# Kernel optimization log

Hardware: AMD Instinct MI355X
Metric: run time of the kernel (lower is better)

## Reference

```python
import jax, jax.numpy as jnp
import numpy as np

B, S, D, F, E = 8, 8192, 256, 1024, 8
ROUTE_KEY = 42  # fixed seed replacing torch's Categorical(...).sample()


def setup_inputs() -> dict:
    key = jax.random.key(0)
    ks = jax.random.split(key, 8)
    scale = 0.02
    return {
        "x": jax.random.normal(ks[0], (B, S, D), dtype=jnp.float32),
        "gate_w": jax.random.normal(ks[1], (D, E), dtype=jnp.float32) * scale,
        "gate_b": jnp.zeros((E,), dtype=jnp.float32),
        "w1": jax.random.normal(ks[2], (E, D, F), dtype=jnp.float32) * scale,
        "b1": jnp.zeros((E, F), dtype=jnp.float32),
        "w2": jax.random.normal(ks[3], (E, F, D), dtype=jnp.float32) * scale,
        "b2": jnp.zeros((E, D), dtype=jnp.float32),
    }


def reference(x, gate_w, gate_b, w1, b1, w2, b2):
    # Gate: logits -> softmax -> sample one expert per token.
    # (softmax is monotonic-preserving for categorical sampling, so sampling
    # from logits directly matches Categorical(softmax(logits)).sample().)
    gate_logits = jnp.einsum("bsd,de->bse", x, gate_w) + gate_b
    chosen = jax.random.categorical(jax.random.key(ROUTE_KEY), gate_logits)  # [B,S] int

    num_experts = w1.shape[0]
    out = jnp.zeros_like(x)
    for e in range(num_experts):  # small fixed expert count
        h = jax.nn.relu(jnp.einsum("bsd,df->bsf", x, w1[e]) + b1[e])
        y = jnp.einsum("bsf,fd->bsd", h, w2[e]) + b2[e]
        # scatter-write rows routed to expert e (dropout is identity in eval)
        out = out + jnp.where((chosen == e)[..., None], y, jnp.zeros((), x.dtype))
    return out
```

## Files before the change

### kernel.cpp

```cpp
#include <hip/hip_runtime.h>
#include <hip/hip_bf16.h>

#define NTOK 65536
#define DD 256
#define FF 1024
#define EE 8
#define BSTRIDE 12288
#define MTILE 128
#define NTILES (BSTRIDE / MTILE)
#define CHUNK_US 16384

typedef short bh8 __attribute__((ext_vector_type(8)));
typedef float f16v __attribute__((ext_vector_type(16)));

__device__ __forceinline__ unsigned rotl32(unsigned v, int d) {
  return (v << d) | (v >> (32 - d));
}

__device__ __forceinline__ unsigned jax_random_bits32(unsigned c0, unsigned c1) {
  const unsigned k0 = 0u, k1 = 42u;
  const unsigned k2 = 0x1BD11BDAu ^ k0 ^ k1;
  unsigned x0 = c0 + k0, x1 = c1 + k1;
#define TFR(r) { x0 += x1; x1 = rotl32(x1, (r)); x1 ^= x0; }
  TFR(13) TFR(15) TFR(26) TFR(6)
  x0 += k1; x1 += k2 + 1u;
  TFR(17) TFR(29) TFR(16) TFR(24)
  x0 += k2; x1 += k0 + 2u;
  TFR(13) TFR(15) TFR(26) TFR(6)
  x0 += k0; x1 += k1 + 3u;
  TFR(17) TFR(29) TFR(16) TFR(24)
  x0 += k1; x1 += k2 + 4u;
  TFR(13) TFR(15) TFR(26) TFR(6)
  x0 += k2; x1 += k0 + 5u;
#undef TFR
  return x0 ^ x1;
}

__device__ __forceinline__ ushort f2bf(float f) {
  union { float f; unsigned u; } c; c.f = f;
  unsigned r = c.u + 0x7fffu + ((c.u >> 16) & 1u);
  return (ushort)(r >> 16);
}

__device__ __forceinline__ unsigned pack2(float a, float b) {
  return (unsigned)f2bf(a) | ((unsigned)f2bf(b) << 16);
}

__global__ __launch_bounds__(1024) void gate_route3(
    const float* __restrict__ x, const float* __restrict__ gw,
    const float* __restrict__ gb, int* __restrict__ counts,
    int* __restrict__ buckets, ushort* __restrict__ xbf) {
  __shared__ float gwt[EE * DD];
  __shared__ int hist[EE], sbase[EE];
  __shared__ unsigned char chs[64];
  __shared__ short lps[64];

  const int tid = threadIdx.x;
  if (tid < EE) hist[tid] = 0;
  for (int i = tid; i < DD * EE; i += 1024) {
    const int d = i >> 3, e = i & 7;
    gwt[e * DD + d] = gw[i];
  }
  __syncthreads();

  const int lane = tid & 63;
  const int wave = tid >> 6;
  const int grp = lane >> 4;
  const int gl = lane & 15;
  const int slot = wave * 4 + grp;
  const int t = blockIdx.x * 64 + slot;

  float acc[EE] = {0.f, 0.f, 0.f, 0.f, 0.f, 0.f, 0.f, 0.f};
  const float* xr = x + (size_t)t * DD;
#pragma unroll
  for (int j = 0; j < 4; ++j) {
    const int d0 = j * 64 + gl * 4;
    const float4 xv = *reinterpret_cast<const float4*>(xr + d0);
    if (xbf != nullptr) {
      ushort4 xb;
      xb.x = f2bf(xv.x); xb.y = f2bf(xv.y); xb.z = f2bf(xv.z); xb.w = f2bf(xv.w);
      *reinterpret_cast<ushort4*>(xbf + (size_t)t * DD + d0) = xb;
    }
#pragma unroll
    for (int e = 0; e < EE; ++e) {
      const float4 g = *reinterpret_cast<const float4*>(&gwt[e * DD + d0]);
      acc[e] = fmaf(xv.x, g.x, acc[e]);
      acc[e] = fmaf(xv.y, g.y, acc[e]);
      acc[e] = fmaf(xv.z, g.z, acc[e]);
      acc[e] = fmaf(xv.w, g.w, acc[e]);
    }
  }
#pragma unroll
  for (int off = 8; off >= 1; off >>= 1)
#pragma unroll
    for (int e = 0; e < EE; ++e) acc[e] += __shfl_xor(acc[e], off);

  const int e = gl & 7;
  float logit = 0.f;
#pragma unroll
  for (int q = 0; q < EE; ++q) logit = (e == q) ? acc[q] : logit;
  logit += gb[e];

  const unsigned bits = jax_random_bits32(0u, (unsigned)(t * EE + e));
  const float f = __uint_as_float((bits >> 9) | 0x3f800000u) - 1.0f;
  const float u = fmaxf(1.17549435e-38f, f);
  float val = -logf(-logf(u)) + logit;
  int idx = e;
#pragma unroll
  for (int off = 4; off > 0; off >>= 1) {
    const float ov = __shfl_xor(val, off);
    const int oi = __shfl_xor(idx, off);
    if (ov > val || (ov == val && oi < idx)) { val = ov; idx = oi; }
  }
  if (gl == 0) {
    const int lp = atomicAdd(&hist[idx], 1);
    chs[slot] = (unsigned char)idx;
    lps[slot] = (short)lp;
  }
  __syncthreads();
  if (tid < EE) sbase[tid] = atomicAdd(&counts[tid], hist[tid]);
  __syncthreads();
  if (tid < 64) {
    const int ee = chs[tid];
    const int p = sbase[ee] + lps[tid];
    if (p < BSTRIDE) buckets[ee * BSTRIDE + p] = blockIdx.x * 64 + tid;
  }
}

__global__ __launch_bounds__(256) void prep_w1s(
    const float* __restrict__ w1, ushort* __restrict__ w1s) {
  __shared__ float ts[64][65];
  const int e = blockIdx.z;
  const int f0 = blockIdx.x * 64, d0 = blockIdx.y * 64;
  const int tx = threadIdx.x, ty = threadIdx.y;
  const float* s = w1 + (size_t)e * DD * FF;
  char* dimg = (char*)(w1s + (size_t)e * 16 * CHUNK_US + blockIdx.x * CHUNK_US);
#pragma unroll
  for (int i = 0; i < 16; ++i)
    ts[ty * 16 + i][tx] = s[(size_t)(d0 + ty * 16 + i) * FF + f0 + tx];
  __syncthreads();
#pragma unroll
  for (int i = 0; i < 16; ++i) {
    const int fl = ty * 16 + i;
    const int byte = ((fl * 512 + (d0 + tx) * 2)) ^ ((fl & 31) << 4);
    *reinterpret_cast<ushort*>(dimg + byte) = f2bf(ts[tx][fl]);
  }
}

__global__ __launch_bounds__(256) void prep_w2s(
    const float* __restrict__ w2, ushort* __restrict__ w2s) {
  __shared__ float ts[64][65];
  const int e = blockIdx.z;
  const int d0 = blockIdx.x * 64, f0 = blockIdx.y * 64;
  const int tx = threadIdx.x, ty = threadIdx.y;
  const float* s = w2 + (size_t)e * FF * DD;
  char* dimg = (char*)(w2s + (size_t)e * 16 * CHUNK_US + blockIdx.y * CHUNK_US);
#pragma unroll
  for (int i = 0; i < 16; ++i)
    ts[ty * 16 + i][tx] = s[(size_t)(f0 + ty * 16 + i) * DD + d0 + tx];
  __syncthreads();
#pragma unroll
  for (int i = 0; i < 16; ++i) {
    const int d = d0 + ty * 16 + i;
    const int byte = ((d * 128 + tx * 2)) ^ ((d & 31) << 4);
    *reinterpret_cast<ushort*>(dimg + byte) = f2bf(ts[tx][ty * 16 + i]);
  }
}

__device__ __forceinline__ void stage32k(const ushort* g, ushort* l, int wid, int lane) {
  const ushort* gs = g + wid * 2048 + lane * 8;
  ushort* ls = l + wid * 2048;
#pragma unroll
  for (int i = 0; i < 4; ++i)
    __builtin_amdgcn_global_load_lds(
        (const __attribute__((address_space(1))) void*)(gs + i * 512),
        (__attribute__((address_space(3))) void*)(ls + i * 512), 16, 0, 0);
}

__global__ __launch_bounds__(512, 2) void ffn_mfma7(
    const ushort* __restrict__ xbf, const ushort* __restrict__ w1s,
    const float* __restrict__ b1, const ushort* __restrict__ w2s,
    const float* __restrict__ b2, const int* __restrict__ counts,
    const int* __restrict__ buckets, float* __restrict__ out) {
  const int e = blockIdx.x & 7;
  const int tile = blockIdx.x >> 3;
  const int cnt = min(counts[e], BSTRIDE);
  const int m0 = tile * MTILE;
  if (m0 >= cnt) return;

  __shared__ ushort W1b[2][CHUNK_US];
  __shared__ ushort W2b[2][CHUNK_US];
  __shared__ ushort Hb[8192];
  __shared__ int toks[MTILE];

  const int tid = threadIdx.x;
  const int lane = tid & 63;
  const int wid = tid >> 6;
  const int l31 = lane & 31;
  const int h = lane >> 5;
  const int g = wid & 1;
  const int j = wid >> 1;
  const int mh = wid >> 2;
  const int dq = wid & 3;

  if (tid < MTILE) {
    const int i = m0 + tid;
    toks[tid] = buckets[e * BSTRIDE + (i < cnt ? i : cnt - 1)];
  }

  const ushort* w1g = w1s + (size_t)e * 16 * CHUNK_US;
  const ushort* w2g = w2s + (size_t)e * 16 * CHUNK_US;

  stage32k(w1g, W1b[0], wid, lane);
  stage32k(w2g, W2b[0], wid, lane);

  const int mx = m0 + j * 32 + l31;
  const int tokx = buckets[e * BSTRIDE + (mx < cnt ? mx : cnt - 1)];
  const ushort* xp = xbf + (size_t)tokx * DD + h * 8;
  bh8 xf[16];
#pragma unroll
  for (int ks = 0; ks < 16; ++ks)
    xf[ks] = *reinterpret_cast<const bh8*>(xp + ks * 16);

  const int fl = g * 32 + l31;
  const int w1x = (fl & 31) << 4;
  __syncthreads();

  f16v yacc[2][2] = {};

#pragma unroll 1
  for (int c = 0; c < 16; ++c) {
    const int p = c & 1;
    if (c < 15) {
      stage32k(w1g + (size_t)(c + 1) * CHUNK_US, W1b[p ^ 1], wid, lane);
      stage32k(w2g + (size_t)(c + 1) * CHUNK_US, W2b[p ^ 1], wid, lane);
    }

    {
      const char* wb = reinterpret_cast<const char*>(W1b[p]);
      f16v hacc = {};
#pragma unroll
      for (int ks = 0; ks < 16; ++ks) {
        const int byte = (fl * 512 + ks * 32 + h * 16) ^ w1x;
        const bh8 a = *reinterpret_cast<const bh8*>(wb + byte);
        hacc = __builtin_amdgcn_mfma_f32_32x32x16_bf16(a, xf[ks], hacc, 0, 0, 0);
      }
      float hv[16];
#pragma unroll
      for (int q = 0; q < 4; ++q) {
        const float4 bv = *reinterpret_cast<const float4*>(
            b1 + e * FF + c * 64 + g * 32 + q * 8 + 4 * h);
        hv[q * 4 + 0] = fmaxf(hacc[q * 4 + 0] + bv.x, 0.f);
        hv[q * 4 + 1] = fmaxf(hacc[q * 4 + 1] + bv.y, 0.f);
        hv[q * 4 + 2] = fmaxf(hacc[q * 4 + 2] + bv.z, 0.f);
        hv[q * 4 + 3] = fmaxf(hacc[q * 4 + 3] + bv.w, 0.f);
      }
      char* hbb = reinterpret_cast<char*>(Hb);
#pragma unroll
      for (int ksl = 0; ksl < 2; ++ksl) {
        const unsigned plo0 = pack2(hv[8 * ksl + 0], hv[8 * ksl + 1]);
        const unsigned plo1 = pack2(hv[8 * ksl + 2], hv[8 * ksl + 3]);
        const unsigned phi0 = pack2(hv[8 * ksl + 4], hv[8 * ksl + 5]);
        const unsigned phi1 = pack2(hv[8 * ksl + 6], hv[8 * ksl + 7]);
        const unsigned r0 = (unsigned)__shfl_xor((int)(h ? plo0 : phi0), 32);
        const unsigned r1 = (unsigned)__shfl_xor((int)(h ? plo1 : phi1), 32);
        uint4 w;
        w.x = h ? r0 : plo0;
        w.y = h ? r1 : plo1;
        w.z = h ? phi0 : r0;
        w.w = h ? phi1 : r1;
        const int M = j, K = g * 2 + ksl;
        *reinterpret_cast<uint4*>(hbb + (M * 4 + K) * 1024 + lane * 16) = w;
      }
    }
    __syncthreads();

    {
      const char* hbb = reinterpret_cast<const char*>(Hb);
      const char* wb = reinterpret_cast<const char*>(W2b[p]);
#pragma unroll
      for (int K = 0; K < 4; ++K) {
        const bh8 a0 = *reinterpret_cast<const bh8*>(
            hbb + ((mh * 2 + 0) * 4 + K) * 1024 + lane * 16);
        const bh8 a1 = *reinterpret_cast<const bh8*>(
            hbb + ((mh * 2 + 1) * 4 + K) * 1024 + lane * 16);
#pragma unroll
        for (int dt = 0; dt < 2; ++dt) {
          const int d = dq * 64 + dt * 32 + l31;
          const int byte = (d * 128 + K * 32 + h * 16) ^ ((d & 31) << 4);
          const bh8 b = *reinterpret_cast<const bh8*>(wb + byte);
          yacc[0][dt] = __builtin_amdgcn_mfma_f32_32x32x16_bf16(a0, b, yacc[0][dt], 0, 0, 0);
          yacc[1][dt] = __builtin_amdgcn_mfma_f32_32x32x16_bf16(a1, b, yacc[1][dt], 0, 0, 0);
        }
      }
    }
    __syncthreads();
  }

#pragma unroll
  for (int mb = 0; mb < 2; ++mb) {
#pragma unroll
    for (int dt = 0; dt < 2; ++dt) {
      const int d = dq * 64 + dt * 32 + l31;
      const float b2v = b2[e * DD + d];
#pragma unroll
      for (int r = 0; r < 16; ++r) {
        const int m = mh * 64 + mb * 32 + (r & 3) + 8 * (r >> 2) + 4 * h;
        if (m0 + m < cnt) {
          out[(size_t)toks[m] * DD + d] = yacc[mb][dt][r] + b2v;
        }
      }
    }
  }
}

__global__ __launch_bounds__(512) void ffn_fp32(
    const float* __restrict__ x, const float* __restrict__ w1,
    const float* __restrict__ b1, const float* __restrict__ w2,
    const float* __restrict__ b2, const int* __restrict__ counts,
    const int* __restrict__ buckets, float* __restrict__ out, int bstride) {
  const int e = blockIdx.y;
  const int cnt = min(counts[e], bstride);
  const int m0 = blockIdx.x * 64;
  if (m0 >= cnt) return;

  __shared__ float Xt[DD][64];
  __shared__ float Ht[64][64];
  __shared__ int toks[64];

  const int tid = threadIdx.x;
  if (tid < 64) {
    const int i = m0 + tid;
    toks[tid] = buckets[e * bstride + (i < cnt ? i : cnt - 1)];
  }
  __syncthreads();

  for (int idx = tid; idx < 64 * (DD / 4); idx += 512) {
    const int r = idx >> 6;
    const int c4 = idx & 63;
    const float4 v = *reinterpret_cast<const float4*>(x + (size_t)toks[r] * DD + c4 * 4);
    Xt[c4 * 4 + 0][r] = v.x;
    Xt[c4 * 4 + 1][r] = v.y;
    Xt[c4 * 4 + 2][r] = v.z;
    Xt[c4 * 4 + 3][r] = v.w;
  }
  __syncthreads();

  const int fg = tid & 15;
  const int mg = tid >> 4;
  const int dc = tid & 63;
  const int mgrp = tid >> 6;

  float yacc[8][4];
#pragma unroll
  for (int i = 0; i < 8; ++i)
#pragma unroll
    for (int jj = 0; jj < 4; ++jj) yacc[i][jj] = 0.f;

  for (int fc0 = 0; fc0 < FF; fc0 += 64) {
    float hacc[2][4];
#pragma unroll
    for (int i = 0; i < 2; ++i)
#pragma unroll
      for (int jj = 0; jj < 4; ++jj) hacc[i][jj] = 0.f;

    const float* w1p = w1 + (size_t)e * DD * FF + fc0 + fg * 4;
    for (int d = 0; d < DD; ++d) {
      const float4 w = *reinterpret_cast<const float4*>(w1p + (size_t)d * FF);
      const float2 xv = *reinterpret_cast<const float2*>(&Xt[d][mg * 2]);
      const float ws[4] = {w.x, w.y, w.z, w.w};
      const float xl[2] = {xv.x, xv.y};
#pragma unroll
      for (int i = 0; i < 2; ++i)
#pragma unroll
        for (int jj = 0; jj < 4; ++jj)
          hacc[i][jj] = fmaf(xl[i], ws[jj], hacc[i][jj]);
    }
#pragma unroll
    for (int jj = 0; jj < 4; ++jj) {
      const float bb = b1[e * FF + fc0 + fg * 4 + jj];
      Ht[fg * 4 + jj][mg * 2 + 0] = fmaxf(hacc[0][jj] + bb, 0.f);
      Ht[fg * 4 + jj][mg * 2 + 1] = fmaxf(hacc[1][jj] + bb, 0.f);
    }
    __syncthreads();

    const float* w2p = w2 + (size_t)e * FF * DD + (size_t)fc0 * DD + dc * 4;
    for (int f = 0; f < 64; ++f) {
      const float4 w = *reinterpret_cast<const float4*>(w2p + (size_t)f * DD);
      const float4 h0 = *reinterpret_cast<const float4*>(&Ht[f][mgrp * 8]);
      const float4 h1 = *reinterpret_cast<const float4*>(&Ht[f][mgrp * 8 + 4]);
      const float hs[8] = {h0.x, h0.y, h0.z, h0.w, h1.x, h1.y, h1.z, h1.w};
      const float ws[4] = {w.x, w.y, w.z, w.w};
#pragma unroll
      for (int i = 0; i < 8; ++i)
#pragma unroll
        for (int jj = 0; jj < 4; ++jj)
          yacc[i][jj] = fmaf(hs[i], ws[jj], yacc[i][jj]);
    }
    __syncthreads();
  }

#pragma unroll
  for (int i = 0; i < 8; ++i) {
    const int r = mgrp * 8 + i;
    if (m0 + r < cnt) {
      float4 o;
      o.x = yacc[i][0] + b2[e * DD + dc * 4 + 0];
      o.y = yacc[i][1] + b2[e * DD + dc * 4 + 1];
      o.z = yacc[i][2] + b2[e * DD + dc * 4 + 2];
      o.w = yacc[i][3] + b2[e * DD + dc * 4 + 3];
      *reinterpret_cast<float4*>(out + (size_t)toks[r] * DD + dc * 4) = o;
    }
  }
}

extern "C" void kernel_launch(void* const* d_in, const int* in_sizes, int n_in,
                              void* d_out, int out_size, void* d_ws, size_t ws_size,
                              hipStream_t stream) {
  const float* x  = (const float*)d_in[0];
  const float* gw = (const float*)d_in[1];
  const float* gb = (const float*)d_in[2];
  const float* w1 = (const float*)d_in[3];
  const float* b1 = (const float*)d_in[4];
  const float* w2 = (const float*)d_in[5];
  const float* b2 = (const float*)d_in[6];
  float* out = (float*)d_out;

  int* counts = (int*)d_ws;
  int* buckets = (int*)((char*)d_ws + 4096);
  ushort* w1s = (ushort*)((char*)d_ws + 524288);
  ushort* w2s = (ushort*)((char*)d_ws + 524288 + 4194304);
  ushort* xbf = (ushort*)((char*)d_ws + 524288 + 2ull * 4194304);
  const size_t need = 524288 + 2ull * 4194304 + (size_t)NTOK * DD * 2;

  hipMemsetAsync(d_ws, 0, 4096, stream);

  if (ws_size >= need) {
    hipLaunchKernelGGL(gate_route3, dim3(NTOK / 64), dim3(1024), 0, stream,
                       x, gw, gb, counts, buckets, xbf);
    hipLaunchKernelGGL(prep_w1s, dim3(FF / 64, DD / 64, EE), dim3(64, 4), 0, stream,
                       w1, w1s);
    hipLaunchKernelGGL(prep_w2s, dim3(DD / 64, FF / 64, EE), dim3(64, 4), 0, stream,
                       w2, w2s);
    hipLaunchKernelGGL(ffn_mfma7, dim3(NTILES * EE), dim3(512), 0, stream,
                       xbf, w1s, b1, w2s, b2, counts, buckets, out);
  } else {
    hipLaunchKernelGGL(gate_route3, dim3(NTOK / 64), dim3(1024), 0, stream,
                       x, gw, gb, counts, buckets, (ushort*)nullptr);
    hipLaunchKernelGGL(ffn_fp32, dim3(NTOK / 64, EE), dim3(512), 0, stream,
                       x, w1, b1, w2, b2, counts, buckets, out, BSTRIDE);
  }
}
```

Measured before the change: 181.9 us.

## Warp-specialize FFN kernel into GEMM1 producer and GEMM2 consumer wave groups

Splits the eight waves into two groups. Four waves compute the first GEMM plus ReLU for chunk c+1 while the other four run the second GEMM for chunk c, passing H through double-buffered shared memory. The row tile shrinks from 128 to 64 tokens, which doubles the number of blocks. b1 is cached in shared memory, and s_setprio is raised around the MFMA loops. Halving the tile also doubles how often each block rereads the weights and limits each GEMM to half the waves, so the overlap gain may be offset by more weight traffic.

```diff
diff --git a/kernel.cpp b/kernel.cpp
--- a/kernel.cpp
+++ b/kernel.cpp
@@ -6,7 +6,7 @@
 #define FF 1024
 #define EE 8
 #define BSTRIDE 12288
-#define MTILE 128
+#define MTILE 64
 #define NTILES (BSTRIDE / MTILE)
 #define CHUNK_US 16384
 
@@ -167,17 +167,17 @@
   }
 }
 
-__device__ __forceinline__ void stage32k(const ushort* g, ushort* l, int wid, int lane) {
-  const ushort* gs = g + wid * 2048 + lane * 8;
-  ushort* ls = l + wid * 2048;
-#pragma unroll
-  for (int i = 0; i < 4; ++i)
+__device__ __forceinline__ void stage32k4(const ushort* g, ushort* l, int widx, int lane) {
+  const ushort* gs = g + widx * 4096 + lane * 8;
+  ushort* ls = l + widx * 4096;
+#pragma unroll
+  for (int i = 0; i < 8; ++i)
     __builtin_amdgcn_global_load_lds(
         (const __attribute__((address_space(1))) void*)(gs + i * 512),
         (__attribute__((address_space(3))) void*)(ls + i * 512), 16, 0, 0);
 }
 
-__global__ __launch_bounds__(512, 2) void ffn_mfma7(
+__global__ __launch_bounds__(512, 2) void ffn_pc(
     const ushort* __restrict__ xbf, const ushort* __restrict__ w1s,
     const float* __restrict__ b1, const ushort* __restrict__ w2s,
     const float* __restrict__ b2, const int* __restrict__ counts,
@@ -190,7 +190,8 @@
 
   __shared__ ushort W1b[2][CHUNK_US];
   __shared__ ushort W2b[2][CHUNK_US];
-  __shared__ ushort Hb[8192];
+  __shared__ ushort Hb[2][4096];
+  __shared__ float Bb[FF];
   __shared__ int toks[MTILE];
 
   const int tid = threadIdx.x;
@@ -198,117 +199,134 @@
   const int wid = tid >> 6;
   const int l31 = lane & 31;
   const int h = lane >> 5;
-  const int g = wid & 1;
-  const int j = wid >> 1;
-  const int mh = wid >> 2;
-  const int dq = wid & 3;
+  const bool isG1 = (wid < 4);
+  const int g = wid >> 1;
+  const int j = wid & 1;
+  const int w2i = wid - 4;
+  const int mh = w2i >> 1;
+  const int dq = w2i & 1;
 
   if (tid < MTILE) {
     const int i = m0 + tid;
     toks[tid] = buckets[e * BSTRIDE + (i < cnt ? i : cnt - 1)];
   }
+  Bb[tid] = b1[e * FF + tid];
+  Bb[tid + 512] = b1[e * FF + 512 + tid];
 
   const ushort* w1g = w1s + (size_t)e * 16 * CHUNK_US;
   const ushort* w2g = w2s + (size_t)e * 16 * CHUNK_US;
 
-  stage32k(w1g, W1b[0], wid, lane);
-  stage32k(w2g, W2b[0], wid, lane);
-
-  const int mx = m0 + j * 32 + l31;
-  const int tokx = buckets[e * BSTRIDE + (mx < cnt ? mx : cnt - 1)];
-  const ushort* xp = xbf + (size_t)tokx * DD + h * 8;
+  if (isG1) {
+    stage32k4(w1g, W1b[0], wid, lane);
+    stage32k4(w1g + CHUNK_US, W1b[1], wid, lane);
+  } else {
+    stage32k4(w2g, W2b[0], w2i, lane);
+  }
+
   bh8 xf[16];
-#pragma unroll
-  for (int ks = 0; ks < 16; ++ks)
-    xf[ks] = *reinterpret_cast<const bh8*>(xp + ks * 16);
+  if (isG1) {
+    const int mxi = m0 + j * 32 + l31;
+    const int tokx = buckets[e * BSTRIDE + (mxi < cnt ? mxi : cnt - 1)];
+    const ushort* xp = xbf + (size_t)tokx * DD + h * 8;
+#pragma unroll
+    for (int ks = 0; ks < 16; ++ks)
+      xf[ks] = *reinterpret_cast<const bh8*>(xp + ks * 16);
+  }
 
   const int fl = g * 32 + l31;
   const int w1x = (fl & 31) << 4;
-  __syncthreads();
-
-  f16v yacc[2][2] = {};
+
+  __syncthreads();
+
+  auto g1_compute = [&](int cc) {
+    const char* wb = reinterpret_cast<const char*>(W1b[cc & 1]);
+    f16v hacc = {};
+    __builtin_amdgcn_s_setprio(1);
+#pragma unroll
+    for (int ks = 0; ks < 16; ++ks) {
+      const int byte = (fl * 512 + ks * 32 + h * 16) ^ w1x;
+      const bh8 a = *reinterpret_cast<const bh8*>(wb + byte);
+      hacc = __builtin_amdgcn_mfma_f32_32x32x16_bf16(a, xf[ks], hacc, 0, 0, 0);
+    }
+    __builtin_amdgcn_s_setprio(0);
+    float hv[16];
+#pragma unroll
+    for (int q = 0; q < 4; ++q) {
+      const float4 bv = *reinterpret_cast<const float4*>(
+          &Bb[cc * 64 + g * 32 + q * 8 + 4 * h]);
+      hv[q * 4 + 0] = fmaxf(hacc[q * 4 + 0] + bv.x, 0.f);
+      hv[q * 4 + 1] = fmaxf(hacc[q * 4 + 1] + bv.y, 0.f);
+      hv[q * 4 + 2] = fmaxf(hacc[q * 4 + 2] + bv.z, 0.f);
+      hv[q * 4 + 3] = fmaxf(hacc[q * 4 + 3] + bv.w, 0.f);
+    }
+    char* hbb = reinterpret_cast<char*>(Hb[cc & 1]);
+#pragma unroll
+    for (int ksl = 0; ksl < 2; ++ksl) {
+      const unsigned plo0 = pack2(hv[8 * ksl + 0], hv[8 * ksl + 1]);
+      const unsigned plo1 = pack2(hv[8 * ksl + 2], hv[8 * ksl + 3]);
+      const unsigned phi0 = pack2(hv[8 * ksl + 4], hv[8 * ksl + 5]);
+      const unsigned phi1 = pack2(hv[8 * ksl + 6], hv[8 * ksl + 7]);
+      const unsigned r0 = (unsigned)__shfl_xor((int)(h ? plo0 : phi0), 32);
+      const unsigned r1 = (unsigned)__shfl_xor((int)(h ? plo1 : phi1), 32);
+      uint4 w;
+      w.x = h ? r0 : plo0;
+      w.y = h ? r1 : plo1;
+      w.z = h ? phi0 : r0;
+      w.w = h ? phi1 : r1;
+      const int K = g * 2 + ksl;
+      *reinterpret_cast<uint4*>(hbb + (j * 4 + K) * 1024 + lane * 16) = w;
+    }
+  };
+
+  f16v yacc[4] = {};
+
+  auto g2_compute = [&](int c) {
+    const char* hbb = reinterpret_cast<const char*>(Hb[c & 1]);
+    const char* wb = reinterpret_cast<const char*>(W2b[c & 1]);
+    __builtin_amdgcn_s_setprio(1);
+#pragma unroll
+    for (int K = 0; K < 4; ++K) {
+      const bh8 hfa = *reinterpret_cast<const bh8*>(
+          hbb + ((mh * 4 + K) * 64 + lane) * 16);
+#pragma unroll
+      for (int dt = 0; dt < 4; ++dt) {
+        const int d = dq * 128 + dt * 32 + l31;
+        const int byte = (d * 128 + K * 32 + h * 16) ^ ((d & 31) << 4);
+        const bh8 b = *reinterpret_cast<const bh8*>(wb + byte);
+        yacc[dt] = __builtin_amdgcn_mfma_f32_32x32x16_bf16(hfa, b, yacc[dt], 0, 0, 0);
+      }
+    }
+    __builtin_amdgcn_s_setprio(0);
+  };
+
+  if (isG1) g1_compute(0);
+  __syncthreads();
 
 #pragma unroll 1
   for (int c = 0; c < 16; ++c) {
-    const int p = c & 1;
-    if (c < 15) {
-      stage32k(w1g + (size_t)(c + 1) * CHUNK_US, W1b[p ^ 1], wid, lane);
-      stage32k(w2g + (size_t)(c + 1) * CHUNK_US, W2b[p ^ 1], wid, lane);
-    }
-
-    {
-      const char* wb = reinterpret_cast<const char*>(W1b[p]);
-      f16v hacc = {};
-#pragma unroll
-      for (int ks = 0; ks < 16; ++ks) {
-        const int byte = (fl * 512 + ks * 32 + h * 16) ^ w1x;
-        const bh8 a = *reinterpret_cast<const bh8*>(wb + byte);
-        hacc = __builtin_amdgcn_mfma_f32_32x32x16_bf16(a, xf[ks], hacc, 0, 0, 0);
-      }
-      float hv[16];
-#pragma unroll
-      for (int q = 0; q < 4; ++q) {
-        const float4 bv = *reinterpret_cast<const float4*>(
-            b1 + e * FF + c * 64 + g * 32 + q * 8 + 4 * h);
-        hv[q * 4 + 0] = fmaxf(hacc[q * 4 + 0] + bv.x, 0.f);
-        hv[q * 4 + 1] = fmaxf(hacc[q * 4 + 1] + bv.y, 0.f);
-        hv[q * 4 + 2] = fmaxf(hacc[q * 4 + 2] + bv.z, 0.f);
-        hv[q * 4 + 3] = fmaxf(hacc[q * 4 + 3] + bv.w, 0.f);
-      }
-      char* hbb = reinterpret_cast<char*>(Hb);
-#pragma unroll
-      for (int ksl = 0; ksl < 2; ++ksl) {
-        const unsigned plo0 = pack2(hv[8 * ksl + 0], hv[8 * ksl + 1]);
-        const unsigned plo1 = pack2(hv[8 * ksl + 2], hv[8 * ksl + 3]);
-        const unsigned phi0 = pack2(hv[8 * ksl + 4], hv[8 * ksl + 5]);
-        const unsigned phi1 = pack2(hv[8 * ksl + 6], hv[8 * ksl + 7]);
-        const unsigned r0 = (unsigned)__shfl_xor((int)(h ? plo0 : phi0), 32);
-        const unsigned r1 = (unsigned)__shfl_xor((int)(h ? plo1 : phi1), 32);
-        uint4 w;
-        w.x = h ? r0 : plo0;
-        w.y = h ? r1 : plo1;
-        w.z = h ? phi0 : r0;
-        w.w = h ? phi1 : r1;
-        const int M = j, K = g * 2 + ksl;
-        *reinterpret_cast<uint4*>(hbb + (M * 4 + K) * 1024 + lane * 16) = w;
-      }
+    if (isG1) {
+      if (c + 2 < 16)
+        stage32k4(w1g + (size_t)(c + 2) * CHUNK_US, W1b[c & 1], wid, lane);
+      if (c + 1 < 16)
+        g1_compute(c + 1);
+    } else {
+      if (c + 1 < 16)
+        stage32k4(w2g + (size_t)(c + 1) * CHUNK_US, W2b[(c + 1) & 1], w2i, lane);
+      g2_compute(c);
     }
     __syncthreads();
-
-    {
-      const char* hbb = reinterpret_cast<const char*>(Hb);
-      const char* wb = reinterpret_cast<const char*>(W2b[p]);
-#pragma unroll
-      for (int K = 0; K < 4; ++K) {
-        const bh8 a0 = *reinterpret_cast<const bh8*>(
-            hbb + ((mh * 2 + 0) * 4 + K) * 1024 + lane * 16);
-        const bh8 a1 = *reinterpret_cast<const bh8*>(
-            hbb + ((mh * 2 + 1) * 4 + K) * 1024 + lane * 16);
-#pragma unroll
-        for (int dt = 0; dt < 2; ++dt) {
-          const int d = dq * 64 + dt * 32 + l31;
-          const int byte = (d * 128 + K * 32 + h * 16) ^ ((d & 31) << 4);
-          const bh8 b = *reinterpret_cast<const bh8*>(wb + byte);
-          yacc[0][dt] = __builtin_amdgcn_mfma_f32_32x32x16_bf16(a0, b, yacc[0][dt], 0, 0, 0);
-          yacc[1][dt] = __builtin_amdgcn_mfma_f32_32x32x16_bf16(a1, b, yacc[1][dt], 0, 0, 0);
-        }
-      }
-    }
-    __syncthreads();
-  }
-
-#pragma unroll
-  for (int mb = 0; mb < 2; ++mb) {
-#pragma unroll
-    for (int dt = 0; dt < 2; ++dt) {
-      const int d = dq * 64 + dt * 32 + l31;
+  }
+
+  if (!isG1) {
+#pragma unroll
+    for (int dt = 0; dt < 4; ++dt) {
+      const int d = dq * 128 + dt * 32 + l31;
       const float b2v = b2[e * DD + d];
 #pragma unroll
       for (int r = 0; r < 16; ++r) {
-        const int m = mh * 64 + mb * 32 + (r & 3) + 8 * (r >> 2) + 4 * h;
-        if (m0 + m < cnt) {
-          out[(size_t)toks[m] * DD + d] = yacc[mb][dt][r] + b2v;
-        }
+        const int m = mh * 32 + (r & 3) + 8 * (r >> 2) + 4 * h;
+        if (m0 + m < cnt)
+          out[(size_t)toks[m] * DD + d] = yacc[dt][r] + b2v;
       }
     }
   }
@@ -442,7 +460,7 @@
                        w1, w1s);
     hipLaunchKernelGGL(prep_w2s, dim3(DD / 64, FF / 64, EE), dim3(64, 4), 0, stream,
                        w2, w2s);
-    hipLaunchKernelGGL(ffn_mfma7, dim3(NTILES * EE), dim3(512), 0, stream,
+    hipLaunchKernelGGL(ffn_pc, dim3(NTILES * EE), dim3(512), 0, stream,
                        xbf, w1s, b1, w2s, b2, counts, buckets, out);
   } else {
     hipLaunchKernelGGL(gate_route3, dim3(NTOK / 64), dim3(1024), 0, stream,
```

Measured after the change: 208.0 us. 1.14x slower.

## Split FFN chunk loop into phased pipeline with staggered prefetch and barriers

Applied to the files above, without the earlier changes.

Restructures the per-chunk loop of the expert FFN kernel into five phases (two half-GEMM1, pack, two half-GEMM2), each separated by a light barrier. The next chunk's weight prefetches are spread across the phases, with explicit vmcnt waits in place of full syncthreads. It also raises wave priority around the MFMA bursts and moves b1 into shared memory. The aim is to overlap global-to-LDS staging with matrix work and cut barrier stalls, at the cost of more barriers and fragile hand-tuned wait counts.

```diff
diff --git a/kernel.cpp b/kernel.cpp
--- a/kernel.cpp
+++ b/kernel.cpp
@@ -12,6 +12,12 @@
 
 typedef short bh8 __attribute__((ext_vector_type(8)));
 typedef float f16v __attribute__((ext_vector_type(16)));
+
+#define PHASE_BAR() do { \
+  asm volatile("s_waitcnt lgkmcnt(0)" ::: "memory"); \
+  __builtin_amdgcn_s_barrier(); \
+  __builtin_amdgcn_sched_barrier(0); \
+} while (0)
 
 __device__ __forceinline__ unsigned rotl32(unsigned v, int d) {
   return (v << d) | (v >> (32 - d));
@@ -176,8 +182,17 @@
         (const __attribute__((address_space(1))) void*)(gs + i * 512),
         (__attribute__((address_space(3))) void*)(ls + i * 512), 16, 0, 0);
 }
-
-__global__ __launch_bounds__(512, 2) void ffn_mfma7(
+__device__ __forceinline__ void stage16k(const ushort* g, ushort* l, int wid, int lane, int half) {
+  const ushort* gs = g + wid * 2048 + lane * 8;
+  ushort* ls = l + wid * 2048;
+#pragma unroll
+  for (int i = 2 * half; i < 2 * half + 2; ++i)
+    __builtin_amdgcn_global_load_lds(
+        (const __attribute__((address_space(1))) void*)(gs + i * 512),
+        (__attribute__((address_space(3))) void*)(ls + i * 512), 16, 0, 0);
+}
+
+__global__ __launch_bounds__(512, 2) void ffn_8p(
     const ushort* __restrict__ xbf, const ushort* __restrict__ w1s,
     const float* __restrict__ b1, const ushort* __restrict__ w2s,
     const float* __restrict__ b2, const int* __restrict__ counts,
@@ -191,6 +206,7 @@
   __shared__ ushort W1b[2][CHUNK_US];
   __shared__ ushort W2b[2][CHUNK_US];
   __shared__ ushort Hb[8192];
+  __shared__ float Bb[FF];
   __shared__ int toks[MTILE];
 
   const int tid = threadIdx.x;
@@ -207,6 +223,8 @@
     const int i = m0 + tid;
     toks[tid] = buckets[e * BSTRIDE + (i < cnt ? i : cnt - 1)];
   }
+  Bb[tid] = b1[e * FF + tid];
+  Bb[tid + 512] = b1[e * FF + 512 + tid];
 
   const ushort* w1g = w1s + (size_t)e * 16 * CHUNK_US;
   const ushort* w2g = w2s + (size_t)e * 16 * CHUNK_US;
@@ -228,73 +246,106 @@
 
   f16v yacc[2][2] = {};
 
+  auto g1_half = [&](const char* wb, bh8* xfp, f16v& hacc, int k0) {
+    __builtin_amdgcn_s_setprio(1);
+#pragma unroll
+    for (int ks = 0; ks < 8; ++ks) {
+      const int kk = k0 + ks;
+      const int byte = (fl * 512 + kk * 32 + h * 16) ^ w1x;
+      const bh8 a = *reinterpret_cast<const bh8*>(wb + byte);
+      hacc = __builtin_amdgcn_mfma_f32_32x32x16_bf16(a, xfp[kk], hacc, 0, 0, 0);
+    }
+    __builtin_amdgcn_s_setprio(0);
+  };
+
+  auto h_pack = [&](int cc, const f16v& hacc) {
+    float hv[16];
+#pragma unroll
+    for (int q = 0; q < 4; ++q) {
+      const float4 bv = *reinterpret_cast<const float4*>(
+          &Bb[cc * 64 + g * 32 + q * 8 + 4 * h]);
+      hv[q * 4 + 0] = fmaxf(hacc[q * 4 + 0] + bv.x, 0.f);
+      hv[q * 4 + 1] = fmaxf(hacc[q * 4 + 1] + bv.y, 0.f);
+      hv[q * 4 + 2] = fmaxf(hacc[q * 4 + 2] + bv.z, 0.f);
+      hv[q * 4 + 3] = fmaxf(hacc[q * 4 + 3] + bv.w, 0.f);
+    }
+    char* hbb = reinterpret_cast<char*>(Hb);
+#pragma unroll
+    for (int ksl = 0; ksl < 2; ++ksl) {
+      const unsigned plo0 = pack2(hv[8 * ksl + 0], hv[8 * ksl + 1]);
+      const unsigned plo1 = pack2(hv[8 * ksl + 2], hv[8 * ksl + 3]);
+      const unsigned phi0 = pack2(hv[8 * ksl + 4], hv[8 * ksl + 5]);
+      const unsigned phi1 = pack2(hv[8 * ksl + 6], hv[8 * ksl + 7]);
+      const unsigned r0 = (unsigned)__shfl_xor((int)(h ? plo0 : phi0), 32);
+      const unsigned r1 = (unsigned)__shfl_xor((int)(h ? plo1 : phi1), 32);
+      uint4 w;
+      w.x = h ? r0 : plo0;
+      w.y = h ? r1 : plo1;
+      w.z = h ? phi0 : r0;
+      w.w = h ? phi1 : r1;
+      const int K = g * 2 + ksl;
+      *reinterpret_cast<uint4*>(hbb + (j * 4 + K) * 1024 + lane * 16) = w;
+    }
+  };
+
+  auto g2_half = [&](const char* wb, int K0) {
+    const char* hbb = reinterpret_cast<const char*>(Hb);
+    __builtin_amdgcn_s_setprio(1);
+#pragma unroll
+    for (int Ki = 0; Ki < 2; ++Ki) {
+      const int K = K0 + Ki;
+      const bh8 a0 = *reinterpret_cast<const bh8*>(
+          hbb + ((mh * 2 + 0) * 4 + K) * 1024 + lane * 16);
+      const bh8 a1 = *reinterpret_cast<const bh8*>(
+          hbb + ((mh * 2 + 1) * 4 + K) * 1024 + lane * 16);
+#pragma unroll
+      for (int dt = 0; dt < 2; ++dt) {
+        const int d = dq * 64 + dt * 32 + l31;
+        const int byte = (d * 128 + K * 32 + h * 16) ^ ((d & 31) << 4);
+        const bh8 b = *reinterpret_cast<const bh8*>(wb + byte);
+        yacc[0][dt] = __builtin_amdgcn_mfma_f32_32x32x16_bf16(a0, b, yacc[0][dt], 0, 0, 0);
+        yacc[1][dt] = __builtin_amdgcn_mfma_f32_32x32x16_bf16(a1, b, yacc[1][dt], 0, 0, 0);
+      }
+    }
+    __builtin_amdgcn_s_setprio(0);
+  };
+
 #pragma unroll 1
-  for (int c = 0; c < 16; ++c) {
+  for (int c = 0; c < 15; ++c) {
     const int p = c & 1;
-    if (c < 15) {
-      stage32k(w1g + (size_t)(c + 1) * CHUNK_US, W1b[p ^ 1], wid, lane);
-      stage32k(w2g + (size_t)(c + 1) * CHUNK_US, W2b[p ^ 1], wid, lane);
-    }
-
-    {
-      const char* wb = reinterpret_cast<const char*>(W1b[p]);
-      f16v hacc = {};
-#pragma unroll
-      for (int ks = 0; ks < 16; ++ks) {
-        const int byte = (fl * 512 + ks * 32 + h * 16) ^ w1x;
-        const bh8 a = *reinterpret_cast<const bh8*>(wb + byte);
-        hacc = __builtin_amdgcn_mfma_f32_32x32x16_bf16(a, xf[ks], hacc, 0, 0, 0);
-      }
-      float hv[16];
-#pragma unroll
-      for (int q = 0; q < 4; ++q) {
-        const float4 bv = *reinterpret_cast<const float4*>(
-            b1 + e * FF + c * 64 + g * 32 + q * 8 + 4 * h);
-        hv[q * 4 + 0] = fmaxf(hacc[q * 4 + 0] + bv.x, 0.f);
-        hv[q * 4 + 1] = fmaxf(hacc[q * 4 + 1] + bv.y, 0.f);
-        hv[q * 4 + 2] = fmaxf(hacc[q * 4 + 2] + bv.z, 0.f);
-        hv[q * 4 + 3] = fmaxf(hacc[q * 4 + 3] + bv.w, 0.f);
-      }
-      char* hbb = reinterpret_cast<char*>(Hb);
-#pragma unroll
-      for (int ksl = 0; ksl < 2; ++ksl) {
-        const unsigned plo0 = pack2(hv[8 * ksl + 0], hv[8 * ksl + 1]);
-        const unsigned plo1 = pack2(hv[8 * ksl + 2], hv[8 * ksl + 3]);
-        const unsigned phi0 = pack2(hv[8 * ksl + 4], hv[8 * ksl + 5]);
-        const unsigned phi1 = pack2(hv[8 * ksl + 6], hv[8 * ksl + 7]);
-        const unsigned r0 = (unsigned)__shfl_xor((int)(h ? plo0 : phi0), 32);
-        const unsigned r1 = (unsigned)__shfl_xor((int)(h ? plo1 : phi1), 32);
-        uint4 w;
-        w.x = h ? r0 : plo0;
-        w.y = h ? r1 : plo1;
-        w.z = h ? phi0 : r0;
-        w.w = h ? phi1 : r1;
-        const int M = j, K = g * 2 + ksl;
-        *reinterpret_cast<uint4*>(hbb + (M * 4 + K) * 1024 + lane * 16) = w;
-      }
-    }
-    __syncthreads();
-
-    {
-      const char* hbb = reinterpret_cast<const char*>(Hb);
-      const char* wb = reinterpret_cast<const char*>(W2b[p]);
-#pragma unroll
-      for (int K = 0; K < 4; ++K) {
-        const bh8 a0 = *reinterpret_cast<const bh8*>(
-            hbb + ((mh * 2 + 0) * 4 + K) * 1024 + lane * 16);
-        const bh8 a1 = *reinterpret_cast<const bh8*>(
-            hbb + ((mh * 2 + 1) * 4 + K) * 1024 + lane * 16);
-#pragma unroll
-        for (int dt = 0; dt < 2; ++dt) {
-          const int d = dq * 64 + dt * 32 + l31;
-          const int byte = (d * 128 + K * 32 + h * 16) ^ ((d & 31) << 4);
-          const bh8 b = *reinterpret_cast<const bh8*>(wb + byte);
-          yacc[0][dt] = __builtin_amdgcn_mfma_f32_32x32x16_bf16(a0, b, yacc[0][dt], 0, 0, 0);
-          yacc[1][dt] = __builtin_amdgcn_mfma_f32_32x32x16_bf16(a1, b, yacc[1][dt], 0, 0, 0);
-        }
-      }
-    }
-    __syncthreads();
+    const char* w1rb = reinterpret_cast<const char*>(W1b[p]);
+    const char* w2rb = reinterpret_cast<const char*>(W2b[p]);
+    f16v hacc = {};
+    stage16k(w1g + (size_t)(c + 1) * CHUNK_US, W1b[p ^ 1], wid, lane, 0);
+    g1_half(w1rb, xf, hacc, 0);
+    PHASE_BAR();
+    stage16k(w1g + (size_t)(c + 1) * CHUNK_US, W1b[p ^ 1], wid, lane, 1);
+    g1_half(w1rb, xf, hacc, 8);
+    PHASE_BAR();
+    stage32k(w2g + (size_t)(c + 1) * CHUNK_US, W2b[p ^ 1], wid, lane);
+    h_pack(c, hacc);
+    asm volatile("s_waitcnt vmcnt(8)" ::: "memory");
+    PHASE_BAR();
+    g2_half(w2rb, 0);
+    PHASE_BAR();
+    g2_half(w2rb, 2);
+    asm volatile("s_waitcnt vmcnt(4)" ::: "memory");
+    PHASE_BAR();
+  }
+  {
+    const char* w1rb = reinterpret_cast<const char*>(W1b[1]);
+    const char* w2rb = reinterpret_cast<const char*>(W2b[1]);
+    f16v hacc = {};
+    g1_half(w1rb, xf, hacc, 0);
+    PHASE_BAR();
+    g1_half(w1rb, xf, hacc, 8);
+    PHASE_BAR();
+    h_pack(15, hacc);
+    asm volatile("s_waitcnt vmcnt(0)" ::: "memory");
+    PHASE_BAR();
+    g2_half(w2rb, 0);
+    PHASE_BAR();
+    g2_half(w2rb, 2);
   }
 
 #pragma unroll
@@ -306,9 +357,8 @@
 #pragma unroll
       for (int r = 0; r < 16; ++r) {
         const int m = mh * 64 + mb * 32 + (r & 3) + 8 * (r >> 2) + 4 * h;
-        if (m0 + m < cnt) {
+        if (m0 + m < cnt)
           out[(size_t)toks[m] * DD + d] = yacc[mb][dt][r] + b2v;
-        }
       }
     }
   }
@@ -442,7 +492,7 @@
                        w1, w1s);
     hipLaunchKernelGGL(prep_w2s, dim3(DD / 64, FF / 64, EE), dim3(64, 4), 0, stream,
                        w2, w2s);
-    hipLaunchKernelGGL(ffn_mfma7, dim3(NTILES * EE), dim3(512), 0, stream,
+    hipLaunchKernelGGL(ffn_8p, dim3(NTILES * EE), dim3(512), 0, stream,
                        xbf, w1s, b1, w2s, b2, counts, buckets, out);
   } else {
     hipLaunchKernelGGL(gate_route3, dim3(NTOK / 64), dim3(1024), 0, stream,
```

After: 205.4 us. +12.9%, slower.
